# Kernel tuning notes

Hardware: AMD Instinct MI355X
Metric: run time of the kernel (lower is better)

The kernel has to match this reference:

```python
import jax, jax.numpy as jnp
import numpy as np

NUM_SPECIES = 7
B, A, F = 1024, 48, 384


def setup_inputs() -> dict:
    key = jax.random.key(0)
    ks = jax.random.split(key, 10)
    species = jax.random.randint(ks[0], (B, A), 0, NUM_SPECIES, dtype=jnp.int32)
    aev = jax.random.normal(ks[1], (B, A, F), dtype=jnp.float32)
    def w(k, shape, fan_in):
        s = 1.0 / np.sqrt(fan_in).astype(np.float32)
        return jax.random.uniform(k, shape, jnp.float32, -s, s)
    return {
        "species": species,
        "aev": aev,
        "W1": w(ks[2], (NUM_SPECIES, 256, 384), 384),
        "b1": w(ks[3], (NUM_SPECIES, 256), 384),
        "W2": w(ks[4], (NUM_SPECIES, 192, 256), 256),
        "b2": w(ks[5], (NUM_SPECIES, 192), 256),
        "W3": w(ks[6], (NUM_SPECIES, 160, 192), 192),
        "b3": w(ks[7], (NUM_SPECIES, 160), 192),
        "W4": w(ks[8], (NUM_SPECIES, 1, 160), 160),
        "b4": w(ks[9], (NUM_SPECIES, 1), 160),
    }


def reference(species, aev, W1, b1, W2, b2, W3, b3, W4, b4):
    # species: [B, A] int, aev: [B, A, 384]
    celu = lambda x: jax.nn.celu(x, alpha=0.1)

    def expert(s):
        # Per-species MLP 384->256->192->160->1 applied to all atoms; selected via mask.
        h = celu(jnp.einsum('baf,hf->bah', aev, W1[s]) + b1[s])
        h = celu(jnp.einsum('bah,gh->bag', h, W2[s]) + b2[s])
        h = celu(jnp.einsum('bag,eg->bae', h, W3[s]) + b3[s])
        return (jnp.einsum('bae,oe->bao', h, W4[s]) + b4[s])[..., 0]  # [B, A]

    atom_energy = jnp.zeros(species.shape, aev.dtype)
    for s in range(NUM_SPECIES):  # fixed small expert loop (hard routing)
        atom_energy = jnp.where(species == s, expert(s), atom_energy)
    # scatter-sum atomic energies into per-molecule energies
    return atom_energy.sum(axis=1)  # [B]
```

## Files before the change

kernel.cpp:

```cpp
#include <hip/hip_runtime.h>
#include <math.h>

#define NSPEC 7
#define NMOL 1024
#define APM 48
#define NATOMS (NMOL * APM)
#define FDIM 384

typedef unsigned short u16;
typedef unsigned int u32;
typedef unsigned long long u64;
typedef __attribute__((ext_vector_type(8))) short short8;
typedef __attribute__((ext_vector_type(4))) float floatx4;

#define W1_ELEMS_PER_S (16 * 12 * 64 * 8)
#define W2_ELEMS_PER_S (12 * 8 * 64 * 8)
#define W3_ELEMS_PER_S (10 * 6 * 64 * 8)

#define BUCKET_BLOCKS (NATOMS / 256)
#define PACK1_BLOCKS (NSPEC * 16)
#define PACK2_BLOCKS (NSPEC * 12)
#define PACK3_BLOCKS (NSPEC * 10)
#define PREP_BLOCKS (BUCKET_BLOCKS + PACK1_BLOCKS + PACK2_BLOCKS + PACK3_BLOCKS)

#define MLP_BLOCKS 775

#define WS_W1_OFF 32
#define WS_W2_OFF (WS_W1_OFF + 1376256)
#define WS_W3_OFF (WS_W2_OFF + 688128)
#define WS_BKT_OFF (WS_W3_OFF + 430080)

#define BUFST 264

__device__ __forceinline__ float celu01(float x) {
    float e = fmaf(0.1f, __expf(x * 10.0f), -0.1f);
    return x > 0.0f ? x : e;
}

__device__ __forceinline__ u16 bfr(float f) {
    u32 u = __float_as_uint(f);
    u += 0x7fffu + ((u >> 16) & 1u);
    return (u16)(u >> 16);
}

__device__ __forceinline__ float bf2f(short s) {
    return __uint_as_float(((u32)(u16)s) << 16);
}

union U8 { short8 v; u16 u[8]; };
union U4 { u64 ll; u16 u[4]; };

template <int KGS, int NTILES>
__device__ __forceinline__ void pack_tile(const float* __restrict__ W,
                                          u16* __restrict__ dst,
                                          int s, int t2, u16* lds) {
    const int K = KGS * 32;
    const int K4 = K / 4;
    int t = threadIdx.x;
    const float* wbase = W + ((size_t)(s * NTILES + t2) * 16) * K;
    for (int i = t; i < 16 * K4; i += 256) {
        int r = i / K4, c = i % K4;
        float4 v = ((const float4*)(wbase + (size_t)r * K))[c];
        u16* d = lds + r * K + c * 4;
        d[0] = bfr(v.x); d[1] = bfr(v.y); d[2] = bfr(v.z); d[3] = bfr(v.w);
    }
    __syncthreads();
    int w = t >> 6, lane = t & 63;
    int n = lane & 15, ks = lane >> 4;
    for (int kg = w; kg < KGS; kg += 4) {
        short8 v = *reinterpret_cast<const short8*>(lds + n * K + kg * 32 + ks * 8);
        *reinterpret_cast<short8*>(
            dst + (((size_t)(s * NTILES + t2) * KGS + kg) * 64 + lane) * 8) = v;
    }
}

__global__ void prep_kernel(const int* __restrict__ species,
                            int* __restrict__ g_cnt, u16* __restrict__ bucket,
                            const float* __restrict__ W1, const float* __restrict__ W2,
                            const float* __restrict__ W3,
                            u16* __restrict__ w1p, u16* __restrict__ w2p,
                            u16* __restrict__ w3p, float* __restrict__ out) {
    __shared__ u16 lds[16 * 384];
    __shared__ int l_cnt[NSPEC];
    __shared__ int l_base[NSPEC];
    int t = threadIdx.x;
    int bx = blockIdx.x;
    if (bx < BUCKET_BLOCKS) {
        if (bx == 0) {
            float4 z = {0.f, 0.f, 0.f, 0.f};
            ((float4*)out)[t] = z;
        }
        if (t < NSPEC) l_cnt[t] = 0;
        __syncthreads();
        int i = bx * 256 + t;
        int s = species[i];
        int lpos = atomicAdd(&l_cnt[s], 1);
        __syncthreads();
        if (t < NSPEC) l_base[t] = atomicAdd(&g_cnt[t], l_cnt[t]);
        __syncthreads();
        bucket[s * NATOMS + l_base[s] + lpos] = (u16)i;
    } else if (bx < BUCKET_BLOCKS + PACK1_BLOCKS) {
        int pid = bx - BUCKET_BLOCKS;
        pack_tile<12, 16>(W1, w1p, pid / 16, pid % 16, lds);
    } else if (bx < BUCKET_BLOCKS + PACK1_BLOCKS + PACK2_BLOCKS) {
        int pid = bx - (BUCKET_BLOCKS + PACK1_BLOCKS);
        pack_tile<8, 12>(W2, w2p, pid / 12, pid % 12, lds);
    } else {
        int pid = bx - (BUCKET_BLOCKS + PACK1_BLOCKS + PACK2_BLOCKS);
        pack_tile<6, 10>(W3, w3p, pid / 10, pid % 10, lds);
    }
}

template <int KGS, int NT, int NBUF>
__device__ __forceinline__ void run_layer(const short8* af0, const short8* af1,
                                          const u16* __restrict__ wsp,
                                          const float* __restrict__ bias,
                                          u16* __restrict__ outbuf, int lane) {
    const int nl = lane & 15, kg4 = lane >> 4;
    const u16* wb = wsp + (size_t)lane * 8;
    short8 b[NBUF][KGS];
#pragma unroll
    for (int p = 0; p < NBUF - 1; ++p)
#pragma unroll
        for (int kg = 0; kg < KGS; ++kg)
            b[p][kg] = *reinterpret_cast<const short8*>(wb + ((size_t)p * KGS + kg) * 512);
#pragma unroll
    for (int t = 0; t < NT; ++t) {
        int pre = t + NBUF - 1;
        if (pre < NT) {
            int slot = pre % NBUF;
#pragma unroll
            for (int kg = 0; kg < KGS; ++kg)
                b[slot][kg] = *reinterpret_cast<const short8*>(wb + ((size_t)pre * KGS + kg) * 512);
        }
        int cur = t % NBUF;
        floatx4 acc0 = {0.f, 0.f, 0.f, 0.f};
        floatx4 acc1 = {0.f, 0.f, 0.f, 0.f};
#pragma unroll
        for (int kg = 0; kg < KGS; ++kg) {
            acc0 = __builtin_amdgcn_mfma_f32_16x16x32_bf16(b[cur][kg], af0[kg], acc0, 0, 0, 0);
            acc1 = __builtin_amdgcn_mfma_f32_16x16x32_bf16(b[cur][kg], af1[kg], acc1, 0, 0, 0);
        }
        floatx4 bn = *reinterpret_cast<const floatx4*>(bias + t * 16 + kg4 * 4);
        U4 p0, p1;
#pragma unroll
        for (int r = 0; r < 4; ++r) {
            p0.u[r] = bfr(celu01(acc0[r] + bn[r]));
            p1.u[r] = bfr(celu01(acc1[r] + bn[r]));
        }
        *reinterpret_cast<u64*>(outbuf + (size_t)nl * BUFST + t * 16 + kg4 * 4) = p0.ll;
        *reinterpret_cast<u64*>(outbuf + (size_t)(16 + nl) * BUFST + t * 16 + kg4 * 4) = p1.ll;
    }
}

template <int KGS>
__device__ __forceinline__ void load_a_lds(const u16* __restrict__ buf,
                                           short8* af0, short8* af1, int lane) {
    int nl = lane & 15, kg4 = lane >> 4;
#pragma unroll
    for (int kg = 0; kg < KGS; ++kg) {
        af0[kg] = *reinterpret_cast<const short8*>(buf + (size_t)nl * BUFST + kg * 32 + kg4 * 8);
        af1[kg] = *reinterpret_cast<const short8*>(buf + (size_t)(16 + nl) * BUFST + kg * 32 + kg4 * 8);
    }
}

__global__ __launch_bounds__(128, 2) void mlp_kernel(
    const float* __restrict__ aev,
    const u16* __restrict__ w1p, const u16* __restrict__ w2p, const u16* __restrict__ w3p,
    const float* __restrict__ b1, const float* __restrict__ b2, const float* __restrict__ b3,
    const float* __restrict__ W4, const float* __restrict__ b4,
    const int* __restrict__ g_cnt, const u16* __restrict__ bucket,
    float* __restrict__ out) {
    int bx = blockIdx.x;
    int s = -1, chunk = 0;
    {
        int acc = 0;
#pragma unroll
        for (int q = 0; q < NSPEC; ++q) {
            int nb = (g_cnt[q] + 63) >> 6;
            if (s < 0 && bx < acc + nb) { s = q; chunk = bx - acc; }
            acc += nb;
        }
        if (s < 0) return;
    }
    int cnt = g_cnt[s];
    int w = threadIdx.x >> 6, lane = threadIdx.x & 63;
    int base = chunk * 64 + w * 32;
    if (base >= cnt) return;

    __shared__ __align__(16) u16 bufs[2][32 * BUFST];
    u16* buf = &bufs[w][0];

    int nl = lane & 15, kg4 = lane >> 4;

    short8 af0[12], af1[12];
    {
        int i0 = base + nl;       if (i0 >= cnt) i0 = cnt - 1;
        int i1 = base + 16 + nl;  if (i1 >= cnt) i1 = cnt - 1;
        int a0 = (int)bucket[s * NATOMS + i0];
        int a1 = (int)bucket[s * NATOMS + i1];
        const float* ar0 = aev + (size_t)a0 * FDIM;
        const float* ar1 = aev + (size_t)a1 * FDIM;
#pragma unroll
        for (int kg = 0; kg < 12; ++kg) {
            const float4* p0 = (const float4*)(ar0 + kg * 32 + kg4 * 8);
            const float4* p1 = (const float4*)(ar1 + kg * 32 + kg4 * 8);
            float4 a = p0[0], b = p0[1];
            float4 c = p1[0], d = p1[1];
            U8 x, y;
            x.u[0] = bfr(a.x); x.u[1] = bfr(a.y); x.u[2] = bfr(a.z); x.u[3] = bfr(a.w);
            x.u[4] = bfr(b.x); x.u[5] = bfr(b.y); x.u[6] = bfr(b.z); x.u[7] = bfr(b.w);
            y.u[0] = bfr(c.x); y.u[1] = bfr(c.y); y.u[2] = bfr(c.z); y.u[3] = bfr(c.w);
            y.u[4] = bfr(d.x); y.u[5] = bfr(d.y); y.u[6] = bfr(d.z); y.u[7] = bfr(d.w);
            af0[kg] = x.v;
            af1[kg] = y.v;
        }
    }
    run_layer<12, 16, 2>(af0, af1, w1p + (size_t)s * W1_ELEMS_PER_S, b1 + s * 256, buf, lane);

    short8 c0[8], c1[8];
    load_a_lds<8>(buf, c0, c1, lane);
    run_layer<8, 12, 3>(c0, c1, w2p + (size_t)s * W2_ELEMS_PER_S, b2 + s * 192, buf, lane);

    short8 d0[6], d1[6];
    load_a_lds<6>(buf, d0, d1, lane);
    run_layer<6, 10, 3>(d0, d1, w3p + (size_t)s * W3_ELEMS_PER_S, b3 + s * 160, buf, lane);

    {
        int m = lane >> 1, q = lane & 1;
        const u16* h = buf + (size_t)m * BUFST + q * 80;
        const float* w4s = W4 + s * 160 + q * 80;
        float p = 0.f;
#pragma unroll
        for (int c = 0; c < 10; ++c) {
            short8 hv = *reinterpret_cast<const short8*>(h + c * 8);
            const float4* wp4 = (const float4*)(w4s + c * 8);
            float4 wa = wp4[0], wb = wp4[1];
            p += bf2f(hv[0]) * wa.x + bf2f(hv[1]) * wa.y + bf2f(hv[2]) * wa.z + bf2f(hv[3]) * wa.w;
            p += bf2f(hv[4]) * wb.x + bf2f(hv[5]) * wb.y + bf2f(hv[6]) * wb.z + bf2f(hv[7]) * wb.w;
        }
        p += __shfl_down(p, 1, 2);
        int idx = base + m;
        if (q == 0 && idx < cnt) {
            int atom = (int)bucket[s * NATOMS + idx];
            atomicAdd(&out[atom / APM], p + b4[s]);
        }
    }
}

extern "C" void kernel_launch(void* const* d_in, const int* in_sizes, int n_in,
                              void* d_out, int out_size, void* d_ws, size_t ws_size,
                              hipStream_t stream) {
    const int* species = (const int*)d_in[0];
    const float* aev = (const float*)d_in[1];
    const float* W1 = (const float*)d_in[2];
    const float* b1 = (const float*)d_in[3];
    const float* W2 = (const float*)d_in[4];
    const float* b2 = (const float*)d_in[5];
    const float* W3 = (const float*)d_in[6];
    const float* b3 = (const float*)d_in[7];
    const float* W4 = (const float*)d_in[8];
    const float* b4 = (const float*)d_in[9];
    float* out = (float*)d_out;

    unsigned char* wsb = (unsigned char*)d_ws;
    int* g_cnt = (int*)wsb;
    u16* w1p = (u16*)(wsb + WS_W1_OFF);
    u16* w2p = (u16*)(wsb + WS_W2_OFF);
    u16* w3p = (u16*)(wsb + WS_W3_OFF);
    u16* bucket = (u16*)(wsb + WS_BKT_OFF);

    hipMemsetAsync(g_cnt, 0, 8 * sizeof(int), stream);

    prep_kernel<<<PREP_BLOCKS, 256, 0, stream>>>(
        species, g_cnt, bucket, W1, W2, W3, w1p, w2p, w3p, out);

    mlp_kernel<<<MLP_BLOCKS, 128, 0, stream>>>(
        aev, w1p, w2p, w3p, b1, b2, b3, W4, b4, g_cnt, bucket, out);
}
```

Baseline: 164.6 us.

## Split output tiles across two waves sharing one 32-atom LDS buffer

Each block now handles 32 atoms instead of 64. Its two waves split the N tiles of every layer (even and odd tiles) rather than each wave taking its own 32 atoms, and they share one LDS activation buffer with __syncthreads between layers. This halves the weight registers and weight loads per wave and doubles the block count, and launch bounds are raised to allow 3 blocks per CU. The atom features are now read with nontemporal loads. Each wave still loads the full A fragments redundantly, and the added block barriers may stall the MFMA pipelines.

```diff
diff --git a/kernel.cpp b/kernel.cpp
--- a/kernel.cpp
+++ b/kernel.cpp
@@ -23,7 +23,7 @@
 #define PACK3_BLOCKS (NSPEC * 10)
 #define PREP_BLOCKS (BUCKET_BLOCKS + PACK1_BLOCKS + PACK2_BLOCKS + PACK3_BLOCKS)
 
-#define MLP_BLOCKS 775
+#define MLP_BLOCKS 1543
 
 #define WS_W1_OFF 32
 #define WS_W2_OFF (WS_W1_OFF + 1376256)
@@ -115,25 +115,26 @@
 __device__ __forceinline__ void run_layer(const short8* af0, const short8* af1,
                                           const u16* __restrict__ wsp,
                                           const float* __restrict__ bias,
-                                          u16* __restrict__ outbuf, int lane) {
+                                          u16* __restrict__ outbuf, int lane, int w) {
+    const int NTL = NT / 2;
     const int nl = lane & 15, kg4 = lane >> 4;
-    const u16* wb = wsp + (size_t)lane * 8;
+    const u16* wb = wsp + (size_t)lane * 8 + (size_t)w * KGS * 512;
     short8 b[NBUF][KGS];
 #pragma unroll
     for (int p = 0; p < NBUF - 1; ++p)
 #pragma unroll
         for (int kg = 0; kg < KGS; ++kg)
-            b[p][kg] = *reinterpret_cast<const short8*>(wb + ((size_t)p * KGS + kg) * 512);
-#pragma unroll
-    for (int t = 0; t < NT; ++t) {
-        int pre = t + NBUF - 1;
-        if (pre < NT) {
+            b[p][kg] = *reinterpret_cast<const short8*>(wb + ((size_t)p * 2 * KGS + kg) * 512);
+#pragma unroll
+    for (int i = 0; i < NTL; ++i) {
+        int pre = i + NBUF - 1;
+        if (pre < NTL) {
             int slot = pre % NBUF;
 #pragma unroll
             for (int kg = 0; kg < KGS; ++kg)
-                b[slot][kg] = *reinterpret_cast<const short8*>(wb + ((size_t)pre * KGS + kg) * 512);
-        }
-        int cur = t % NBUF;
+                b[slot][kg] = *reinterpret_cast<const short8*>(wb + ((size_t)pre * 2 * KGS + kg) * 512);
+        }
+        int cur = i % NBUF;
         floatx4 acc0 = {0.f, 0.f, 0.f, 0.f};
         floatx4 acc1 = {0.f, 0.f, 0.f, 0.f};
 #pragma unroll
@@ -141,6 +142,7 @@
             acc0 = __builtin_amdgcn_mfma_f32_16x16x32_bf16(b[cur][kg], af0[kg], acc0, 0, 0, 0);
             acc1 = __builtin_amdgcn_mfma_f32_16x16x32_bf16(b[cur][kg], af1[kg], acc1, 0, 0, 0);
         }
+        int t = 2 * i + w;
         floatx4 bn = *reinterpret_cast<const floatx4*>(bias + t * 16 + kg4 * 4);
         U4 p0, p1;
 #pragma unroll
@@ -164,7 +166,7 @@
     }
 }
 
-__global__ __launch_bounds__(128, 2) void mlp_kernel(
+__global__ __launch_bounds__(128, 3) void mlp_kernel(
     const float* __restrict__ aev,
     const u16* __restrict__ w1p, const u16* __restrict__ w2p, const u16* __restrict__ w3p,
     const float* __restrict__ b1, const float* __restrict__ b2, const float* __restrict__ b3,
@@ -177,7 +179,7 @@
         int acc = 0;
 #pragma unroll
         for (int q = 0; q < NSPEC; ++q) {
-            int nb = (g_cnt[q] + 63) >> 6;
+            int nb = (g_cnt[q] + 31) >> 5;
             if (s < 0 && bx < acc + nb) { s = q; chunk = bx - acc; }
             acc += nb;
         }
@@ -185,11 +187,9 @@
     }
     int cnt = g_cnt[s];
     int w = threadIdx.x >> 6, lane = threadIdx.x & 63;
-    int base = chunk * 64 + w * 32;
-    if (base >= cnt) return;
-
-    __shared__ __align__(16) u16 bufs[2][32 * BUFST];
-    u16* buf = &bufs[w][0];
+    int base = chunk * 32;
+
+    __shared__ __align__(16) u16 buf[32 * BUFST];
 
     int nl = lane & 15, kg4 = lane >> 4;
 
@@ -203,47 +203,57 @@
         const float* ar1 = aev + (size_t)a1 * FDIM;
 #pragma unroll
         for (int kg = 0; kg < 12; ++kg) {
-            const float4* p0 = (const float4*)(ar0 + kg * 32 + kg4 * 8);
-            const float4* p1 = (const float4*)(ar1 + kg * 32 + kg4 * 8);
-            float4 a = p0[0], b = p0[1];
-            float4 c = p1[0], d = p1[1];
+            const floatx4* p0 = (const floatx4*)(ar0 + kg * 32 + kg4 * 8);
+            const floatx4* p1 = (const floatx4*)(ar1 + kg * 32 + kg4 * 8);
+            floatx4 va = __builtin_nontemporal_load(p0);
+            floatx4 vb = __builtin_nontemporal_load(p0 + 1);
+            floatx4 vc = __builtin_nontemporal_load(p1);
+            floatx4 vd = __builtin_nontemporal_load(p1 + 1);
             U8 x, y;
-            x.u[0] = bfr(a.x); x.u[1] = bfr(a.y); x.u[2] = bfr(a.z); x.u[3] = bfr(a.w);
-            x.u[4] = bfr(b.x); x.u[5] = bfr(b.y); x.u[6] = bfr(b.z); x.u[7] = bfr(b.w);
-            y.u[0] = bfr(c.x); y.u[1] = bfr(c.y); y.u[2] = bfr(c.z); y.u[3] = bfr(c.w);
-            y.u[4] = bfr(d.x); y.u[5] = bfr(d.y); y.u[6] = bfr(d.z); y.u[7] = bfr(d.w);
+            x.u[0] = bfr(va[0]); x.u[1] = bfr(va[1]); x.u[2] = bfr(va[2]); x.u[3] = bfr(va[3]);
+            x.u[4] = bfr(vb[0]); x.u[5] = bfr(vb[1]); x.u[6] = bfr(vb[2]); x.u[7] = bfr(vb[3]);
+            y.u[0] = bfr(vc[0]); y.u[1] = bfr(vc[1]); y.u[2] = bfr(vc[2]); y.u[3] = bfr(vc[3]);
+            y.u[4] = bfr(vd[0]); y.u[5] = bfr(vd[1]); y.u[6] = bfr(vd[2]); y.u[7] = bfr(vd[3]);
             af0[kg] = x.v;
             af1[kg] = y.v;
         }
     }
-    run_layer<12, 16, 2>(af0, af1, w1p + (size_t)s * W1_ELEMS_PER_S, b1 + s * 256, buf, lane);
+    run_layer<12, 16, 2>(af0, af1, w1p + (size_t)s * W1_ELEMS_PER_S, b1 + s * 256, buf, lane, w);
+    __syncthreads();
 
     short8 c0[8], c1[8];
     load_a_lds<8>(buf, c0, c1, lane);
-    run_layer<8, 12, 3>(c0, c1, w2p + (size_t)s * W2_ELEMS_PER_S, b2 + s * 192, buf, lane);
+    __syncthreads();
+    run_layer<8, 12, 3>(c0, c1, w2p + (size_t)s * W2_ELEMS_PER_S, b2 + s * 192, buf, lane, w);
+    __syncthreads();
 
     short8 d0[6], d1[6];
     load_a_lds<6>(buf, d0, d1, lane);
-    run_layer<6, 10, 3>(d0, d1, w3p + (size_t)s * W3_ELEMS_PER_S, b3 + s * 160, buf, lane);
+    __syncthreads();
+    run_layer<6, 10, 3>(d0, d1, w3p + (size_t)s * W3_ELEMS_PER_S, b3 + s * 160, buf, lane, w);
+    __syncthreads();
 
     {
         int m = lane >> 1, q = lane & 1;
-        const u16* h = buf + (size_t)m * BUFST + q * 80;
-        const float* w4s = W4 + s * 160 + q * 80;
-        float p = 0.f;
-#pragma unroll
-        for (int c = 0; c < 10; ++c) {
-            short8 hv = *reinterpret_cast<const short8*>(h + c * 8);
-            const float4* wp4 = (const float4*)(w4s + c * 8);
-            float4 wa = wp4[0], wb = wp4[1];
-            p += bf2f(hv[0]) * wa.x + bf2f(hv[1]) * wa.y + bf2f(hv[2]) * wa.z + bf2f(hv[3]) * wa.w;
-            p += bf2f(hv[4]) * wb.x + bf2f(hv[5]) * wb.y + bf2f(hv[6]) * wb.z + bf2f(hv[7]) * wb.w;
-        }
-        p += __shfl_down(p, 1, 2);
-        int idx = base + m;
-        if (q == 0 && idx < cnt) {
-            int atom = (int)bucket[s * NATOMS + idx];
-            atomicAdd(&out[atom / APM], p + b4[s]);
+        if (m < 16) {
+            int ai = w * 16 + m;
+            const u16* h = buf + (size_t)ai * BUFST + q * 80;
+            const float* w4s = W4 + s * 160 + q * 80;
+            float p = 0.f;
+#pragma unroll
+            for (int c = 0; c < 10; ++c) {
+                short8 hv = *reinterpret_cast<const short8*>(h + c * 8);
+                const float4* wp4 = (const float4*)(w4s + c * 8);
+                float4 wa = wp4[0], wb = wp4[1];
+                p += bf2f(hv[0]) * wa.x + bf2f(hv[1]) * wa.y + bf2f(hv[2]) * wa.z + bf2f(hv[3]) * wa.w;
+                p += bf2f(hv[4]) * wb.x + bf2f(hv[5]) * wb.y + bf2f(hv[6]) * wb.z + bf2f(hv[7]) * wb.w;
+            }
+            p += __shfl_down(p, 1, 2);
+            int idx = base + ai;
+            if (q == 0 && idx < cnt) {
+                int atom = (int)bucket[s * NATOMS + idx];
+                atomicAdd(&out[atom / APM], p + b4[s]);
+            }
         }
     }
 }
```

After: 222.6 us. 35.2% more time.

## Shrink MLP work unit to one wave per 16-atom tile

Applied to the files above, without the earlier changes.

Each block becomes a single 64-lane wave processing 16 atoms instead of two waves with 32 atoms each, so the grid grows about fourfold. The layer loop now splits K into halves with a three-slot weight prefetch ring and a single accumulator. The final dot product is spread over four lanes per atom. The goal is more parallelism and lower register pressure for better latency hiding. The cost is that each weight fragment now feeds half as many MFMAs, roughly doubling weight traffic per atom.

```diff
diff --git a/kernel.cpp b/kernel.cpp
--- a/kernel.cpp
+++ b/kernel.cpp
@@ -23,7 +23,7 @@
 #define PACK3_BLOCKS (NSPEC * 10)
 #define PREP_BLOCKS (BUCKET_BLOCKS + PACK1_BLOCKS + PACK2_BLOCKS + PACK3_BLOCKS)
 
-#define MLP_BLOCKS 775
+#define MLP_BLOCKS 3078
 
 #define WS_W1_OFF 32
 #define WS_W2_OFF (WS_W1_OFF + 1376256)
@@ -111,60 +111,56 @@
     }
 }
 
-template <int KGS, int NT, int NBUF>
-__device__ __forceinline__ void run_layer(const short8* af0, const short8* af1,
-                                          const u16* __restrict__ wsp,
-                                          const float* __restrict__ bias,
-                                          u16* __restrict__ outbuf, int lane) {
+template <int KGS, int NT>
+__device__ __forceinline__ void run_layer16(const short8* af,
+                                            const u16* __restrict__ wsp,
+                                            const float* __restrict__ bias,
+                                            u16* __restrict__ outbuf, int lane) {
+    const int HALF = KGS / 2;
+    const int NH = NT * 2;
     const int nl = lane & 15, kg4 = lane >> 4;
     const u16* wb = wsp + (size_t)lane * 8;
-    short8 b[NBUF][KGS];
-#pragma unroll
-    for (int p = 0; p < NBUF - 1; ++p)
-#pragma unroll
-        for (int kg = 0; kg < KGS; ++kg)
-            b[p][kg] = *reinterpret_cast<const short8*>(wb + ((size_t)p * KGS + kg) * 512);
-#pragma unroll
-    for (int t = 0; t < NT; ++t) {
-        int pre = t + NBUF - 1;
-        if (pre < NT) {
-            int slot = pre % NBUF;
-#pragma unroll
-            for (int kg = 0; kg < KGS; ++kg)
-                b[slot][kg] = *reinterpret_cast<const short8*>(wb + ((size_t)pre * KGS + kg) * 512);
-        }
-        int cur = t % NBUF;
-        floatx4 acc0 = {0.f, 0.f, 0.f, 0.f};
-        floatx4 acc1 = {0.f, 0.f, 0.f, 0.f};
-#pragma unroll
-        for (int kg = 0; kg < KGS; ++kg) {
-            acc0 = __builtin_amdgcn_mfma_f32_16x16x32_bf16(b[cur][kg], af0[kg], acc0, 0, 0, 0);
-            acc1 = __builtin_amdgcn_mfma_f32_16x16x32_bf16(b[cur][kg], af1[kg], acc1, 0, 0, 0);
-        }
-        floatx4 bn = *reinterpret_cast<const floatx4*>(bias + t * 16 + kg4 * 4);
-        U4 p0, p1;
-#pragma unroll
-        for (int r = 0; r < 4; ++r) {
-            p0.u[r] = bfr(celu01(acc0[r] + bn[r]));
-            p1.u[r] = bfr(celu01(acc1[r] + bn[r]));
-        }
-        *reinterpret_cast<u64*>(outbuf + (size_t)nl * BUFST + t * 16 + kg4 * 4) = p0.ll;
-        *reinterpret_cast<u64*>(outbuf + (size_t)(16 + nl) * BUFST + t * 16 + kg4 * 4) = p1.ll;
+    short8 b[3][HALF];
+#pragma unroll
+    for (int p = 0; p < 2; ++p)
+#pragma unroll
+        for (int k = 0; k < HALF; ++k)
+            b[p][k] = *reinterpret_cast<const short8*>(wb + ((size_t)p * HALF + k) * 512);
+    floatx4 acc = {0.f, 0.f, 0.f, 0.f};
+#pragma unroll
+    for (int h = 0; h < NH; ++h) {
+        int pre = h + 2;
+        if (pre < NH) {
+#pragma unroll
+            for (int k = 0; k < HALF; ++k)
+                b[pre % 3][k] = *reinterpret_cast<const short8*>(wb + ((size_t)pre * HALF + k) * 512);
+        }
+#pragma unroll
+        for (int k = 0; k < HALF; ++k)
+            acc = __builtin_amdgcn_mfma_f32_16x16x32_bf16(b[h % 3][k], af[(h & 1) * HALF + k], acc, 0, 0, 0);
+        if (h & 1) {
+            int t = h >> 1;
+            floatx4 bn = *reinterpret_cast<const floatx4*>(bias + t * 16 + kg4 * 4);
+            U4 pk;
+#pragma unroll
+            for (int r = 0; r < 4; ++r)
+                pk.u[r] = bfr(celu01(acc[r] + bn[r]));
+            *reinterpret_cast<u64*>(outbuf + (size_t)nl * BUFST + t * 16 + kg4 * 4) = pk.ll;
+            acc = (floatx4){0.f, 0.f, 0.f, 0.f};
+        }
     }
 }
 
 template <int KGS>
-__device__ __forceinline__ void load_a_lds(const u16* __restrict__ buf,
-                                           short8* af0, short8* af1, int lane) {
+__device__ __forceinline__ void load_a16(const u16* __restrict__ buf,
+                                         short8* af, int lane) {
     int nl = lane & 15, kg4 = lane >> 4;
 #pragma unroll
-    for (int kg = 0; kg < KGS; ++kg) {
-        af0[kg] = *reinterpret_cast<const short8*>(buf + (size_t)nl * BUFST + kg * 32 + kg4 * 8);
-        af1[kg] = *reinterpret_cast<const short8*>(buf + (size_t)(16 + nl) * BUFST + kg * 32 + kg4 * 8);
-    }
-}
-
-__global__ __launch_bounds__(128, 2) void mlp_kernel(
+    for (int kg = 0; kg < KGS; ++kg)
+        af[kg] = *reinterpret_cast<const short8*>(buf + (size_t)nl * BUFST + kg * 32 + kg4 * 8);
+}
+
+__global__ __launch_bounds__(64, 3) void mlp_kernel(
     const float* __restrict__ aev,
     const u16* __restrict__ w1p, const u16* __restrict__ w2p, const u16* __restrict__ w3p,
     const float* __restrict__ b1, const float* __restrict__ b2, const float* __restrict__ b3,
@@ -177,69 +173,60 @@
         int acc = 0;
 #pragma unroll
         for (int q = 0; q < NSPEC; ++q) {
-            int nb = (g_cnt[q] + 63) >> 6;
+            int nb = (g_cnt[q] + 15) >> 4;
             if (s < 0 && bx < acc + nb) { s = q; chunk = bx - acc; }
             acc += nb;
         }
         if (s < 0) return;
     }
     int cnt = g_cnt[s];
-    int w = threadIdx.x >> 6, lane = threadIdx.x & 63;
-    int base = chunk * 64 + w * 32;
-    if (base >= cnt) return;
-
-    __shared__ __align__(16) u16 bufs[2][32 * BUFST];
-    u16* buf = &bufs[w][0];
+    int lane = threadIdx.x & 63;
+    int base = chunk * 16;
+
+    __shared__ __align__(16) u16 buf[16 * BUFST];
 
     int nl = lane & 15, kg4 = lane >> 4;
 
-    short8 af0[12], af1[12];
+    short8 af[12];
     {
-        int i0 = base + nl;       if (i0 >= cnt) i0 = cnt - 1;
-        int i1 = base + 16 + nl;  if (i1 >= cnt) i1 = cnt - 1;
+        int i0 = base + nl;  if (i0 >= cnt) i0 = cnt - 1;
         int a0 = (int)bucket[s * NATOMS + i0];
-        int a1 = (int)bucket[s * NATOMS + i1];
         const float* ar0 = aev + (size_t)a0 * FDIM;
-        const float* ar1 = aev + (size_t)a1 * FDIM;
 #pragma unroll
         for (int kg = 0; kg < 12; ++kg) {
             const float4* p0 = (const float4*)(ar0 + kg * 32 + kg4 * 8);
-            const float4* p1 = (const float4*)(ar1 + kg * 32 + kg4 * 8);
             float4 a = p0[0], b = p0[1];
-            float4 c = p1[0], d = p1[1];
-            U8 x, y;
+            U8 x;
             x.u[0] = bfr(a.x); x.u[1] = bfr(a.y); x.u[2] = bfr(a.z); x.u[3] = bfr(a.w);
             x.u[4] = bfr(b.x); x.u[5] = bfr(b.y); x.u[6] = bfr(b.z); x.u[7] = bfr(b.w);
-            y.u[0] = bfr(c.x); y.u[1] = bfr(c.y); y.u[2] = bfr(c.z); y.u[3] = bfr(c.w);
-            y.u[4] = bfr(d.x); y.u[5] = bfr(d.y); y.u[6] = bfr(d.z); y.u[7] = bfr(d.w);
-            af0[kg] = x.v;
-            af1[kg] = y.v;
-        }
-    }
-    run_layer<12, 16, 2>(af0, af1, w1p + (size_t)s * W1_ELEMS_PER_S, b1 + s * 256, buf, lane);
-
-    short8 c0[8], c1[8];
-    load_a_lds<8>(buf, c0, c1, lane);
-    run_layer<8, 12, 3>(c0, c1, w2p + (size_t)s * W2_ELEMS_PER_S, b2 + s * 192, buf, lane);
-
-    short8 d0[6], d1[6];
-    load_a_lds<6>(buf, d0, d1, lane);
-    run_layer<6, 10, 3>(d0, d1, w3p + (size_t)s * W3_ELEMS_PER_S, b3 + s * 160, buf, lane);
+            af[kg] = x.v;
+        }
+    }
+    run_layer16<12, 16>(af, w1p + (size_t)s * W1_ELEMS_PER_S, b1 + s * 256, buf, lane);
+
+    short8 c[8];
+    load_a16<8>(buf, c, lane);
+    run_layer16<8, 12>(c, w2p + (size_t)s * W2_ELEMS_PER_S, b2 + s * 192, buf, lane);
+
+    short8 d[6];
+    load_a16<6>(buf, d, lane);
+    run_layer16<6, 10>(d, w3p + (size_t)s * W3_ELEMS_PER_S, b3 + s * 160, buf, lane);
 
     {
-        int m = lane >> 1, q = lane & 1;
-        const u16* h = buf + (size_t)m * BUFST + q * 80;
-        const float* w4s = W4 + s * 160 + q * 80;
+        int m = lane >> 2, q = lane & 3;
+        const u16* h = buf + (size_t)m * BUFST + q * 40;
+        const float* w4s = W4 + s * 160 + q * 40;
         float p = 0.f;
 #pragma unroll
-        for (int c = 0; c < 10; ++c) {
-            short8 hv = *reinterpret_cast<const short8*>(h + c * 8);
-            const float4* wp4 = (const float4*)(w4s + c * 8);
+        for (int cc = 0; cc < 5; ++cc) {
+            short8 hv = *reinterpret_cast<const short8*>(h + cc * 8);
+            const float4* wp4 = (const float4*)(w4s + cc * 8);
             float4 wa = wp4[0], wb = wp4[1];
             p += bf2f(hv[0]) * wa.x + bf2f(hv[1]) * wa.y + bf2f(hv[2]) * wa.z + bf2f(hv[3]) * wa.w;
             p += bf2f(hv[4]) * wb.x + bf2f(hv[5]) * wb.y + bf2f(hv[6]) * wb.z + bf2f(hv[7]) * wb.w;
         }
-        p += __shfl_down(p, 1, 2);
+        p += __shfl_down(p, 2, 4);
+        p += __shfl_down(p, 1, 4);
         int idx = base + m;
         if (q == 0 && idx < cnt) {
             int atom = (int)bucket[s * NATOMS + idx];
@@ -275,6 +262,6 @@
     prep_kernel<<<PREP_BLOCKS, 256, 0, stream>>>(
         species, g_cnt, bucket, W1, W2, W3, w1p, w2p, w3p, out);
 
-    mlp_kernel<<<MLP_BLOCKS, 128, 0, stream>>>(
+    mlp_kernel<<<MLP_BLOCKS, 64, 0, stream>>>(
         aev, w1p, w2p, w3p, b1, b2, b3, W4, b4, g_cnt, bucket, out);
 }
```

Measured after the change: 181.3 us. 1.1x slower.
